# Kernel optimization log

Hardware: AMD Instinct MI355X
Metric: run time of the kernel (lower is better)

Reference implementation:

```python
import jax, jax.numpy as jnp
import numpy as np

D_MODEL = 1024
D_STATE = 16
D_CONV = 4
EXPAND = 2
INNER = EXPAND * D_MODEL          # 2048
DT_RANK = (D_MODEL + 15) // 16     # 64 ('auto' heuristic)
BATCH = 1
SEQLEN = 2048
DT_MIN, DT_MAX, DT_FLOOR = 1e-3, 1e-1, 1e-4


def setup_inputs() -> dict:
    key = jax.random.key(0)
    ks = jax.random.split(key, 8)
    hidden_states = jax.random.normal(ks[0], (BATCH, SEQLEN, D_MODEL), jnp.float32)
    W_in = jax.random.normal(ks[1], (2 * INNER, D_MODEL), jnp.float32) * (D_MODEL ** -0.5)
    conv_w = jax.random.normal(ks[2], (INNER, D_CONV), jnp.float32) * 0.02
    conv_b = jnp.zeros((INNER,), jnp.float32)
    W_x = jax.random.normal(ks[3], (DT_RANK + 2 * D_STATE, INNER), jnp.float32) * (INNER ** -0.5)
    dt_init_std = DT_RANK ** -0.5
    W_dt = jax.random.uniform(ks[4], (INNER, DT_RANK), jnp.float32, -dt_init_std, dt_init_std)
    # dt_bias = inverse-softplus of dt sampled log-uniform in [dt_min, dt_max]
    dt = jnp.exp(jax.random.uniform(ks[5], (INNER,), jnp.float32)
                 * (np.log(DT_MAX) - np.log(DT_MIN)) + np.log(DT_MIN))
    dt = jnp.clip(dt, DT_FLOOR)
    dt_bias = dt + jnp.log(-jnp.expm1(-dt))
    A_log = jax.random.normal(ks[6], (INNER, D_STATE), jnp.float32) * 0.5
    D_skip = jnp.ones((INNER,), jnp.float32)
    W_out = jax.random.normal(ks[7], (D_MODEL, INNER), jnp.float32) * (INNER ** -0.5)
    return dict(hidden_states=hidden_states, W_in=W_in, conv_w=conv_w, conv_b=conv_b,
                W_x=W_x, W_dt=W_dt, dt_bias=dt_bias, A_log=A_log, D_skip=D_skip, W_out=W_out)


def _silu(x):
    return x * jax.nn.sigmoid(x)


def reference(hidden_states, W_in, conv_w, conv_b, W_x, W_dt, dt_bias, A_log, D_skip, W_out):
    # in_proj: (B, L, d_model) -> (B, L, 2*inner), split into x-branch and gate
    xz = hidden_states @ W_in.T
    proj, gate = jnp.split(xz, 2, axis=-1)

    # depthwise causal conv along L with silu activation
    xc = proj.transpose(0, 2, 1)                       # (B, inner, L)
    kernel = conv_w[:, None, :]                        # (inner, 1, d_conv)
    conv = jax.lax.conv_general_dilated(
        xc, kernel, window_strides=(1,), padding=[(D_CONV - 1, 0)],
        dimension_numbers=('NCH', 'OIH', 'NCH'), feature_group_count=INNER)
    conv = _silu(conv + conv_b[None, :, None])         # (B, inner, L)
    u = conv.transpose(0, 2, 1)                        # (B, L, inner)

    # x_proj -> low-rank dt, B, C per-token
    projt = u @ W_x.T                                  # (B, L, dt_rank + 2*N)
    dt_lr, Bp, Cp = jnp.split(projt, [DT_RANK, DT_RANK + D_STATE], axis=-1)
    delta = jax.nn.softplus(dt_lr @ W_dt.T + dt_bias)  # (B, L, inner)

    # selective scan: h_t = exp(delta*A) h_{t-1} + delta*B_t*u_t
    A = -jnp.exp(A_log)                                # (inner, N)
    dA = jnp.exp(jnp.einsum('bld,dn->lbdn', delta, A))            # (L,B,inner,N)
    dBu = jnp.einsum('bld,bln,bld->lbdn', delta, Bp, u)           # (L,B,inner,N)

    def step(h, inp):
        dA_t, dBu_t = inp
        h = dA_t * h + dBu_t
        return h, h

    h0 = jnp.zeros((hidden_states.shape[0], INNER, D_STATE), u.dtype)
    _, hs = jax.lax.scan(step, h0, (dA, dBu))          # (L,B,inner,N)

    y = jnp.einsum('lbdn,bln->bld', hs, Cp)            # (B, L, inner)
    y = y + D_skip * u                                 # D skip connection
    y = y * _silu(gate)                                # gated output
    return y @ W_out.T                                 # (B, L, d_model)
```

## Files before the change

kernel.cpp:

```cpp
#include <hip/hip_runtime.h>
#include <hip/hip_bf16.h>

#define SEQLEN 2048
#define DMODEL 1024
#define INNER  2048
#define DSTATE 16
#define DTRANK 64
#define NPROJ  96
#define NPAD   128
#define CHUNK  32
#define NCH    64

typedef __attribute__((ext_vector_type(8))) short bf16x8;
typedef __attribute__((ext_vector_type(4))) float f32x4;

__device__ __forceinline__ float softplusf(float x) {
    return (x > 20.f) ? x : log1pf(__expf(x));
}
__device__ __forceinline__ unsigned short f2bf(float x) {
    unsigned u = __float_as_uint(x);
    return (unsigned short)((u + 0x7FFF + ((u >> 16) & 1)) >> 16);
}
__device__ __forceinline__ float bf2f(unsigned short x) {
    return __uint_as_float((unsigned)x << 16);
}
__device__ __forceinline__ void gload_lds16(const void* g, void* l) {
    __builtin_amdgcn_global_load_lds(
        (__attribute__((address_space(1))) const unsigned int*)g,
        (__attribute__((address_space(3))) unsigned int*)l,
        16, 0, 0);
}
__device__ __forceinline__ void cvt8(const float* __restrict__ in,
                                     unsigned short* __restrict__ out, int i) {
    float4 a = ((const float4*)in)[2 * i];
    float4 b = ((const float4*)in)[2 * i + 1];
    uint4 v;
    v.x = f2bf(a.x) | ((unsigned)f2bf(a.y) << 16);
    v.y = f2bf(a.z) | ((unsigned)f2bf(a.w) << 16);
    v.z = f2bf(b.x) | ((unsigned)f2bf(b.y) << 16);
    v.w = f2bf(b.z) | ((unsigned)f2bf(b.w) << 16);
    ((uint4*)out)[i] = v;
}

__global__ __launch_bounds__(256)
void cvt_all(const float* __restrict__ hidden, const float* __restrict__ W_in,
             const float* __restrict__ W_out, const float* __restrict__ W_dt,
             const float* __restrict__ W_x,
             unsigned short* __restrict__ hid_b, unsigned short* __restrict__ Win_b,
             unsigned short* __restrict__ Wout_b, unsigned short* __restrict__ Wdt_b,
             unsigned short* __restrict__ Wx_b)
{
    int i = blockIdx.x * 256 + threadIdx.x;
    if (i < 262144) { cvt8(hidden, hid_b, i); return; }
    i -= 262144;
    if (i < 524288) { cvt8(W_in, Win_b, i); return; }
    i -= 524288;
    if (i < 262144) { cvt8(W_out, Wout_b, i); return; }
    i -= 262144;
    if (i < 16384)  { cvt8(W_dt, Wdt_b, i); return; }
    i -= 16384;
    if (i < 32768) {
        int row = i >> 8;
        if (row < NPROJ) cvt8(W_x, Wx_b, i);
        else ((uint4*)Wx_b)[i] = make_uint4(0, 0, 0, 0);
    }
}

template<int BM, int BN, int EPI>
__global__ __launch_bounds__(256)
void gemm_bf16(const unsigned short* __restrict__ A, const int lda,
               const unsigned short* __restrict__ B, const int ldb,
               void* __restrict__ Cv, const int ldc, const long long zCstride,
               const int K, const int kspan, const float* __restrict__ bias)
{
    constexpr int FM = BM / 32;
    constexpr int FN = BN / 32;
    __shared__ alignas(16) short As[BM * 32];
    __shared__ alignas(16) short Bs[BN * 32];

    const int tid  = threadIdx.x;
    const int wave = tid >> 6;
    const int lane = tid & 63;
    const long long row0 = (long long)blockIdx.y * BM;
    const long long col0 = (long long)blockIdx.x * BN;
    const int wm = (wave >> 1) * (BM / 2);
    const int wn = (wave & 1) * (BN / 2);
    const int kstart = blockIdx.z * kspan;
    const int kend   = min(K, kstart + kspan);

    f32x4 acc[FM][FN] = {};

    const int srow = tid >> 2;
    const int scol = (tid & 3) * 8;
    const unsigned short* gA = A + (row0 + srow) * lda + scol;
    const unsigned short* gB = B + (col0 + srow) * ldb + scol;

    const int fr = lane & 15;
    const int fk = (lane >> 4) * 8;

    for (int kt = kstart; kt < kend; kt += 32) {
#pragma unroll
        for (int r = 0; r < BM; r += 64)
            gload_lds16(gA + (long long)r * lda + kt, &As[r * 32 + tid * 8]);
#pragma unroll
        for (int r = 0; r < BN; r += 64)
            gload_lds16(gB + (long long)r * ldb + kt, &Bs[r * 32 + tid * 8]);
        __syncthreads();

        bf16x8 af[FM], bfr[FN];
#pragma unroll
        for (int mi = 0; mi < FM; ++mi)
            af[mi] = *(const bf16x8*)&As[(wm + mi * 16 + fr) * 32 + fk];
#pragma unroll
        for (int ni = 0; ni < FN; ++ni)
            bfr[ni] = *(const bf16x8*)&Bs[(wn + ni * 16 + fr) * 32 + fk];
#pragma unroll
        for (int mi = 0; mi < FM; ++mi)
#pragma unroll
            for (int ni = 0; ni < FN; ++ni)
                acc[mi][ni] = __builtin_amdgcn_mfma_f32_16x16x32_bf16(
                    af[mi], bfr[ni], acc[mi][ni], 0, 0, 0);
        __syncthreads();
    }

    const int cr = (lane >> 4) * 4;
#pragma unroll
    for (int mi = 0; mi < FM; ++mi)
#pragma unroll
        for (int ni = 0; ni < FN; ++ni) {
            long long rbase = row0 + wm + mi * 16 + cr;
            long long col   = col0 + wn + ni * 16 + fr;
#pragma unroll
            for (int r = 0; r < 4; ++r) {
                long long idx = (rbase + r) * ldc + col;
                if (EPI == 0) {
                    ((float*)Cv)[(long long)blockIdx.z * zCstride + idx] = acc[mi][ni][r];
                } else if (EPI == 1) {
                    ((unsigned short*)Cv)[idx] = f2bf(acc[mi][ni][r]);
                } else {
                    ((unsigned short*)Cv)[idx] = f2bf(softplusf(acc[mi][ni][r] + bias[col]));
                }
            }
        }
}

__global__ __launch_bounds__(256)
void conv_silu_kernel(const unsigned short* __restrict__ xz_b, const float* __restrict__ cw,
                      const float* __restrict__ cb, unsigned short* __restrict__ u_b)
{
    int i = blockIdx.x * 256 + threadIdx.x;
    int l  = i >> 9;
    int dq = i & 511;
    int d  = dq * 4;
    float4 wv[4];
#pragma unroll
    for (int k = 0; k < 4; ++k) wv[k] = ((const float4*)cw)[d + k];
    float4 acc = ((const float4*)cb)[dq];
#pragma unroll
    for (int j = 0; j < 4; ++j) {
        int ls = l - 3 + j;
        if (ls >= 0) {
            ushort4 x = *(const ushort4*)&xz_b[(long long)ls * 4096 + d];
            acc.x = fmaf(((const float*)&wv[0])[j], bf2f(x.x), acc.x);
            acc.y = fmaf(((const float*)&wv[1])[j], bf2f(x.y), acc.y);
            acc.z = fmaf(((const float*)&wv[2])[j], bf2f(x.z), acc.z);
            acc.w = fmaf(((const float*)&wv[3])[j], bf2f(x.w), acc.w);
        }
    }
    float4 r;
    r.x = acc.x / (1.f + __expf(-acc.x));
    r.y = acc.y / (1.f + __expf(-acc.y));
    r.z = acc.z / (1.f + __expf(-acc.z));
    r.w = acc.w / (1.f + __expf(-acc.w));
    uint2 p;
    p.x = f2bf(r.x) | ((unsigned)f2bf(r.y) << 16);
    p.y = f2bf(r.z) | ((unsigned)f2bf(r.w) << 16);
    ((uint2*)u_b)[i] = p;
}

__global__ __launch_bounds__(256)
void reduce_part(const float* __restrict__ part, float* __restrict__ projt,
                 unsigned short* __restrict__ projt_b)
{
    int i = blockIdx.x * 256 + threadIdx.x;
    float s = 0.f;
#pragma unroll
    for (int z = 0; z < 8; ++z) s += part[(long long)z * SEQLEN * NPAD + i];
    projt[i] = s;
    projt_b[i] = f2bf(s);
}

__global__ __launch_bounds__(256)
void scan_phase1(const unsigned short* __restrict__ delta_bf,
                 const unsigned short* __restrict__ u_b,
                 const float* __restrict__ projt, const float* __restrict__ A_log,
                 float* __restrict__ Sloc, float* __restrict__ sumd)
{
    __shared__ float Bsh[CHUNK][16];
    const int d  = blockIdx.x * 256 + threadIdx.x;
    const int c  = blockIdx.y;
    const int l0 = c * CHUNK;
    for (int i = threadIdx.x; i < CHUNK * 16; i += 256) {
        int l = i >> 4, j = i & 15;
        Bsh[l][j] = projt[(l0 + l) * NPAD + DTRANK + j];
    }
    __syncthreads();

    float A2[DSTATE];
#pragma unroll
    for (int n = 0; n < DSTATE; ++n)
        A2[n] = -__expf(A_log[d * DSTATE + n]) * 1.4426950408889634f;

    float dl[CHUNK], du[CHUNK];
#pragma unroll
    for (int t = 0; t < CHUNK; ++t) {
        int l = l0 + t;
        float dv = bf2f(delta_bf[l * INNER + d]);
        dl[t] = dv;
        du[t] = dv * bf2f(u_b[l * INNER + d]);
    }

    float h[DSTATE];
#pragma unroll
    for (int n = 0; n < DSTATE; ++n) h[n] = 0.f;
    float sd = 0.f;

#pragma unroll
    for (int t = 0; t < CHUNK; ++t) {
        sd += dl[t];
#pragma unroll
        for (int n = 0; n < DSTATE; ++n) {
            float dA = exp2f(dl[t] * A2[n]);
            h[n] = fmaf(dA, h[n], du[t] * Bsh[t][n]);
        }
    }
#pragma unroll
    for (int n = 0; n < DSTATE; ++n)
        Sloc[(c * INNER + d) * DSTATE + n] = h[n];
    sumd[c * INNER + d] = sd;
}

__global__ __launch_bounds__(256)
void scan_phase2(float* __restrict__ S, const float* __restrict__ sumd,
                 const float* __restrict__ A_log)
{
    int i = blockIdx.x * 256 + threadIdx.x;
    int d = i >> 4;
    float A2 = -__expf(A_log[i]) * 1.4426950408889634f;
    float H = 0.f;
#pragma unroll
    for (int c = 0; c < NCH; ++c) {
        float s = S[c * INNER * DSTATE + i];
        float P = exp2f(A2 * sumd[c * INNER + d]);
        S[c * INNER * DSTATE + i] = H;
        H = fmaf(P, H, s);
    }
}

__global__ __launch_bounds__(256)
void scan_phase3(const unsigned short* __restrict__ delta_bf,
                 const unsigned short* __restrict__ u_b,
                 const float* __restrict__ projt, const float* __restrict__ A_log,
                 const float* __restrict__ Hinit, const unsigned short* __restrict__ xz_b,
                 const float* __restrict__ D_skip, unsigned short* __restrict__ ybf)
{
    __shared__ float BC[CHUNK][32];
    const int d  = blockIdx.x * 256 + threadIdx.x;
    const int c  = blockIdx.y;
    const int l0 = c * CHUNK;
    for (int i = threadIdx.x; i < CHUNK * 32; i += 256) {
        int l = i >> 5, j = i & 31;
        BC[l][j] = projt[(l0 + l) * NPAD + DTRANK + j];
    }
    __syncthreads();

    float A2[DSTATE];
#pragma unroll
    for (int n = 0; n < DSTATE; ++n)
        A2[n] = -__expf(A_log[d * DSTATE + n]) * 1.4426950408889634f;

    float dl[CHUNK], uv[CHUNK];
#pragma unroll
    for (int t = 0; t < CHUNK; ++t) {
        int l = l0 + t;
        dl[t] = bf2f(delta_bf[l * INNER + d]);
        uv[t] = bf2f(u_b[l * INNER + d]);
    }

    float h[DSTATE];
#pragma unroll
    for (int n = 0; n < DSTATE; ++n)
        h[n] = Hinit[(c * INNER + d) * DSTATE + n];
    const float Dd = D_skip[d];

#pragma unroll
    for (int t = 0; t < CHUNK; ++t) {
        int l = l0 + t;
        float du = dl[t] * uv[t];
        float y = 0.f;
#pragma unroll
        for (int n = 0; n < DSTATE; ++n) {
            float dA = exp2f(dl[t] * A2[n]);
            h[n] = fmaf(dA, h[n], du * BC[t][n]);
            y = fmaf(h[n], BC[t][16 + n], y);
        }
        float yv = fmaf(Dd, uv[t], y);
        float g = bf2f(xz_b[(long long)l * 4096 + 2048 + d]);
        float sg = g / (1.f + __expf(-g));
        ybf[l * INNER + d] = f2bf(yv * sg);
    }
}

extern "C" void kernel_launch(void* const* d_in, const int* in_sizes, int n_in,
                              void* d_out, int out_size, void* d_ws, size_t ws_size,
                              hipStream_t stream)
{
    const float* hidden  = (const float*)d_in[0];
    const float* W_in    = (const float*)d_in[1];
    const float* conv_w  = (const float*)d_in[2];
    const float* conv_b  = (const float*)d_in[3];
    const float* W_x     = (const float*)d_in[4];
    const float* W_dt    = (const float*)d_in[5];
    const float* dt_bias = (const float*)d_in[6];
    const float* A_log   = (const float*)d_in[7];
    const float* D_skip  = (const float*)d_in[8];
    const float* W_out   = (const float*)d_in[9];
    float* out = (float*)d_out;

    char* base = (char*)d_ws;
    unsigned short* xz_b    = (unsigned short*)(base + 0);
    unsigned short* hid_b   = (unsigned short*)(base + 16777216);
    unsigned short* Win_b   = (unsigned short*)(base + 20971520);
    unsigned short* u_b     = (unsigned short*)(base + 16777216);
    float*          part    = (float*)(base + 25165824);
    float*          Sloc    = (float*)(base + 25165824);
    unsigned short* dlt_b   = (unsigned short*)(base + 37748736);
    unsigned short* y_b     = (unsigned short*)(base + 46137344);
    float*          projt   = (float*)(base + 54525952);
    unsigned short* projt_b = (unsigned short*)(base + 55574528);
    unsigned short* Wout_b  = (unsigned short*)(base + 56098816);
    unsigned short* Wx_b    = (unsigned short*)(base + 60293120);
    unsigned short* Wdt_b   = (unsigned short*)(base + 60817408);
    float*          sumd    = (float*)(base + 61079552);

    cvt_all<<<4289, 256, 0, stream>>>(hidden, W_in, W_out, W_dt, W_x,
                                      hid_b, Win_b, Wout_b, Wdt_b, Wx_b);

    gemm_bf16<128, 128, 1><<<dim3(32, 16, 1), 256, 0, stream>>>(
        hid_b, DMODEL, Win_b, DMODEL, xz_b, 4096, 0, DMODEL, DMODEL, nullptr);

    conv_silu_kernel<<<SEQLEN * 512 / 256, 256, 0, stream>>>(xz_b, conv_w, conv_b, u_b);

    gemm_bf16<128, 128, 0><<<dim3(1, 16, 8), 256, 0, stream>>>(
        u_b, INNER, Wx_b, INNER, part, NPAD, (long long)SEQLEN * NPAD,
        INNER, INNER / 8, nullptr);
    reduce_part<<<SEQLEN * NPAD / 256, 256, 0, stream>>>(part, projt, projt_b);

    gemm_bf16<128, 128, 2><<<dim3(16, 16, 1), 256, 0, stream>>>(
        projt_b, NPAD, Wdt_b, DTRANK, dlt_b, INNER, 0, DTRANK, DTRANK, dt_bias);

    scan_phase1<<<dim3(INNER / 256, NCH), 256, 0, stream>>>(dlt_b, u_b, projt, A_log, Sloc, sumd);
    scan_phase2<<<(INNER * DSTATE) / 256, 256, 0, stream>>>(Sloc, sumd, A_log);
    scan_phase3<<<dim3(INNER / 256, NCH), 256, 0, stream>>>(dlt_b, u_b, projt, A_log,
                                                            Sloc, xz_b, D_skip, y_b);

    gemm_bf16<128, 64, 0><<<dim3(16, 16, 1), 256, 0, stream>>>(
        y_b, INNER, Wout_b, INNER, out, DMODEL, 0, INNER, INNER, nullptr);
}
```

Baseline: 191.5 us.

## Double GEMM K-tile with XOR-swizzled LDS, remap block order, split-K out_proj

The bf16 MFMA GEMM now stages 64-wide K tiles instead of 32, halving the number of barrier pairs per K loop. It XOR-swizzles the LDS chunk layout so fragment reads avoid bank conflicts. Block IDs are remapped in groups of eight, likely to spread neighbouring tiles across XCDs or improve L2 locality. The output projection is split over K into two partial buffers, with a new reduction kernel to raise the block count. The cost is double the LDS use, an extra launch, and extra global traffic for the partial sums.

Measured after the change: 173.0 us. -9.7%, faster.

```diff
diff --git a/kernel.cpp b/kernel.cpp
--- a/kernel.cpp
+++ b/kernel.cpp
@@ -75,14 +75,21 @@
 {
     constexpr int FM = BM / 32;
     constexpr int FN = BN / 32;
-    __shared__ alignas(16) short As[BM * 32];
-    __shared__ alignas(16) short Bs[BN * 32];
+    __shared__ alignas(16) short As[BM * 64];
+    __shared__ alignas(16) short Bs[BN * 64];
 
     const int tid  = threadIdx.x;
     const int wave = tid >> 6;
     const int lane = tid & 63;
-    const long long row0 = (long long)blockIdx.y * BM;
-    const long long col0 = (long long)blockIdx.x * BN;
+
+    int bid = blockIdx.y * gridDim.x + blockIdx.x;
+    const int q = (gridDim.x * gridDim.y) >> 3;
+    bid = (bid & 7) * q + (bid >> 3);
+    const int bx = bid % gridDim.x;
+    const int by = bid / gridDim.x;
+
+    const long long row0 = (long long)by * BM;
+    const long long col0 = (long long)bx * BN;
     const int wm = (wave >> 1) * (BM / 2);
     const int wn = (wave & 1) * (BN / 2);
     const int kstart = blockIdx.z * kspan;
@@ -90,40 +97,47 @@
 
     f32x4 acc[FM][FN] = {};
 
-    const int srow = tid >> 2;
-    const int scol = (tid & 3) * 8;
-    const unsigned short* gA = A + (row0 + srow) * lda + scol;
-    const unsigned short* gB = B + (col0 + srow) * ldb + scol;
+    const int srow   = tid >> 3;
+    const int schunk = (tid & 7) ^ (srow & 7);
+    const unsigned short* gA = A + (row0 + srow) * lda + schunk * 8;
+    const unsigned short* gB = B + (col0 + srow) * ldb + schunk * 8;
+    short* lA = &As[srow * 64 + (tid & 7) * 8];
+    short* lB = &Bs[srow * 64 + (tid & 7) * 8];
 
     const int fr = lane & 15;
-    const int fk = (lane >> 4) * 8;
-
-    for (int kt = kstart; kt < kend; kt += 32) {
-#pragma unroll
-        for (int r = 0; r < BM; r += 64)
-            gload_lds16(gA + (long long)r * lda + kt, &As[r * 32 + tid * 8]);
-#pragma unroll
-        for (int r = 0; r < BN; r += 64)
-            gload_lds16(gB + (long long)r * ldb + kt, &Bs[r * 32 + tid * 8]);
+    const int hi = lane >> 4;
+    const int rb = fr & 7;
+
+    for (int kt = kstart; kt < kend; kt += 64) {
+#pragma unroll
+        for (int r = 0; r < BM; r += 32)
+            gload_lds16(gA + (long long)r * lda + kt, lA + r * 64);
+#pragma unroll
+        for (int r = 0; r < BN; r += 32)
+            gload_lds16(gB + (long long)r * ldb + kt, lB + r * 64);
         __syncthreads();
 
-        bf16x8 af[FM], bfr[FN];
-#pragma unroll
-        for (int mi = 0; mi < FM; ++mi)
-            af[mi] = *(const bf16x8*)&As[(wm + mi * 16 + fr) * 32 + fk];
-#pragma unroll
-        for (int ni = 0; ni < FN; ++ni)
-            bfr[ni] = *(const bf16x8*)&Bs[(wn + ni * 16 + fr) * 32 + fk];
-#pragma unroll
-        for (int mi = 0; mi < FM; ++mi)
+#pragma unroll
+        for (int half = 0; half < 2; ++half) {
+            const int kc = (((half << 2) + hi) ^ rb) * 8;
+            bf16x8 af[FM], bfr[FN];
+#pragma unroll
+            for (int mi = 0; mi < FM; ++mi)
+                af[mi] = *(const bf16x8*)&As[(wm + mi * 16 + fr) * 64 + kc];
 #pragma unroll
             for (int ni = 0; ni < FN; ++ni)
-                acc[mi][ni] = __builtin_amdgcn_mfma_f32_16x16x32_bf16(
-                    af[mi], bfr[ni], acc[mi][ni], 0, 0, 0);
+                bfr[ni] = *(const bf16x8*)&Bs[(wn + ni * 16 + fr) * 64 + kc];
+#pragma unroll
+            for (int mi = 0; mi < FM; ++mi)
+#pragma unroll
+                for (int ni = 0; ni < FN; ++ni)
+                    acc[mi][ni] = __builtin_amdgcn_mfma_f32_16x16x32_bf16(
+                        af[mi], bfr[ni], acc[mi][ni], 0, 0, 0);
+        }
         __syncthreads();
     }
 
-    const int cr = (lane >> 4) * 4;
+    const int cr = hi * 4;
 #pragma unroll
     for (int mi = 0; mi < FM; ++mi)
 #pragma unroll
@@ -142,6 +156,16 @@
                 }
             }
         }
+}
+
+__global__ __launch_bounds__(256)
+void reduce_out(const float* __restrict__ part, float* __restrict__ out)
+{
+    int i = blockIdx.x * 256 + threadIdx.x;
+    float4 a = ((const float4*)part)[i];
+    float4 b = ((const float4*)part)[i + SEQLEN * DMODEL / 4];
+    a.x += b.x; a.y += b.y; a.z += b.z; a.w += b.w;
+    ((float4*)out)[i] = a;
 }
 
 __global__ __launch_bounds__(256)
@@ -342,6 +366,7 @@
     unsigned short* Wx_b    = (unsigned short*)(base + 60293120);
     unsigned short* Wdt_b   = (unsigned short*)(base + 60817408);
     float*          sumd    = (float*)(base + 61079552);
+    float*          opart   = (float*)(base + 61603840);
 
     cvt_all<<<4289, 256, 0, stream>>>(hidden, W_in, W_out, W_dt, W_x,
                                       hid_b, Win_b, Wout_b, Wdt_b, Wx_b);
@@ -364,6 +389,8 @@
     scan_phase3<<<dim3(INNER / 256, NCH), 256, 0, stream>>>(dlt_b, u_b, projt, A_log,
                                                             Sloc, xz_b, D_skip, y_b);
 
-    gemm_bf16<128, 64, 0><<<dim3(16, 16, 1), 256, 0, stream>>>(
-        y_b, INNER, Wout_b, INNER, out, DMODEL, 0, INNER, INNER, nullptr);
-}
+    gemm_bf16<128, 64, 0><<<dim3(16, 16, 2), 256, 0, stream>>>(
+        y_b, INNER, Wout_b, INNER, opart, DMODEL, (long long)SEQLEN * DMODEL,
+        INNER, INNER / 2, nullptr);
+    reduce_out<<<SEQLEN * DMODEL / 1024, 256, 0, stream>>>(opart, out);
+}
```
